# Optimization experiments

Measured on AMD Instinct MI355X. Metric: run time of the kernel, lower is better.

## Reference

```python
import jax, jax.numpy as jnp
import numpy as np

# Faithful emulation of SQBnBLinear: SmoothQuant rescale fused with
# bnb Linear8bitLt (threshold=0.0 => no fp16 outlier path):
#   w_sq = weight / scales ; x_sq = x * scales
#   row-wise absmax int8 quantization of both x (per token) and w (per out row)
#   int8 GEMM, then dequant with (ax * aw / 127^2), plus bias / scales.

B, S, D = 4, 2048, 4096

def setup_inputs() -> dict:
    key = jax.random.key(0)
    k1, k2, k3, k4 = jax.random.split(key, 4)
    x = jax.random.normal(k1, (B, S, D), dtype=jnp.float32)
    weight = jax.random.normal(k2, (D, D), dtype=jnp.float32) * 0.02
    bias = jax.random.normal(k3, (D,), dtype=jnp.float32) * 0.02
    # SmoothQuant scales are positive per-input-channel factors
    scales = jax.random.uniform(k4, (D,), dtype=jnp.float32, minval=0.5, maxval=2.0)
    return {"x": x, "weight": weight, "bias": bias, "scales": scales}

def _quantize_rowwise(t):
    # symmetric per-row (last-dim) absmax int8 quantization
    absmax = jnp.max(jnp.abs(t), axis=-1, keepdims=True)
    absmax = jnp.maximum(absmax, 1e-8)
    q = jnp.clip(jnp.round(t * (127.0 / absmax)), -127.0, 127.0)
    return q, absmax

def reference(x, weight, bias, scales):
    # __init__: fold SmoothQuant scales into weight and bias
    w_sq = weight / scales            # [out, in] / [in]
    b_sq = bias / scales              # valid because in_features == out_features
    # forward: rescale input (mul_ by scales)
    x_sq = x * scales                 # [B, S, in]
    # LLM.int8() with threshold=0.0: pure int8 path
    qx, ax = _quantize_rowwise(x_sq)  # qx [B,S,in], ax [B,S,1]
    qw, aw = _quantize_rowwise(w_sq)  # qw [out,in], aw [out,1]
    acc = jnp.einsum('bsi,oi->bso', qx, qw)  # int accumulate (emulated in fp32)
    out = acc * (ax / 127.0) * (aw[:, 0] / 127.0) + b_sq
    return out
```

## Files before the change

kernel.cpp:

```cpp
#include <hip/hip_runtime.h>
#include <stdint.h>

#define DDIM 4096
#define MTOK 8192

typedef __attribute__((ext_vector_type(4))) int i32x4;

__device__ __forceinline__ void async16(const void* g, void* l) {
    __builtin_amdgcn_global_load_lds(
        (const __attribute__((address_space(1))) unsigned int*)g,
        (__attribute__((address_space(3))) unsigned int*)l,
        16, 0, 0);
}

template <int MODE>
__global__ __launch_bounds__(256) void quant_rows(
    const float* __restrict__ src, const float* __restrict__ scales,
    signed char* __restrict__ q, float* __restrict__ srow,
    const float* __restrict__ bias, float* __restrict__ bq)
{
    __shared__ float red[4];
    const int row = blockIdx.x;
    const int tid = threadIdx.x;
    const float4* s4 = (const float4*)scales;
    const float4* x4 = (const float4*)(src + (size_t)row * DDIM);

    float4 v[4];
    float am = 0.0f;
#pragma unroll
    for (int j = 0; j < 4; ++j) {
        float4 a = x4[tid + j * 256];
        float4 s = s4[tid + j * 256];
        float4 r;
        if (MODE == 0) { r.x = a.x * s.x; r.y = a.y * s.y; r.z = a.z * s.z; r.w = a.w * s.w; }
        else           { r.x = a.x / s.x; r.y = a.y / s.y; r.z = a.z / s.z; r.w = a.w / s.w; }
        v[j] = r;
        am = fmaxf(am, fmaxf(fmaxf(fabsf(r.x), fabsf(r.y)),
                             fmaxf(fabsf(r.z), fabsf(r.w))));
    }
#pragma unroll
    for (int off = 32; off > 0; off >>= 1)
        am = fmaxf(am, __shfl_xor(am, off, 64));
    if ((tid & 63) == 0) red[tid >> 6] = am;
    __syncthreads();
    am = fmaxf(fmaxf(red[0], red[1]), fmaxf(red[2], red[3]));
    am = fmaxf(am, 1e-8f);

    const float sc = 127.0f / am;
    uint32_t* qrow = (uint32_t*)(q + (size_t)row * DDIM);
#pragma unroll
    for (int j = 0; j < 4; ++j) {
        int q0 = (int)fminf(127.0f, fmaxf(-127.0f, rintf(v[j].x * sc)));
        int q1 = (int)fminf(127.0f, fmaxf(-127.0f, rintf(v[j].y * sc)));
        int q2 = (int)fminf(127.0f, fmaxf(-127.0f, rintf(v[j].z * sc)));
        int q3 = (int)fminf(127.0f, fmaxf(-127.0f, rintf(v[j].w * sc)));
        qrow[tid + j * 256] = (uint32_t)(q0 & 0xff) | ((uint32_t)(q1 & 0xff) << 8) |
                              ((uint32_t)(q2 & 0xff) << 16) | ((uint32_t)(q3 & 0xff) << 24);
    }
    if (tid == 0) {
        srow[row] = am * (1.0f / 127.0f);
        if (MODE == 1) bq[row] = bias[row] / scales[row];
    }
}

__global__ __launch_bounds__(256) void gemm_i8(
    const signed char* __restrict__ qx, const signed char* __restrict__ qw,
    const float* __restrict__ sx, const float* __restrict__ sw,
    const float* __restrict__ bq, float* __restrict__ out)
{
    __shared__ __align__(16) signed char sA[128 * 64];
    __shared__ __align__(16) signed char sB[128 * 64];

    const int K = DDIM, N = DDIM;
    const int tid  = threadIdx.x;
    const int bm   = blockIdx.y;
    const int bn   = blockIdx.x;
    const int wave = tid >> 6;
    const int lane = tid & 63;
    const int wm   = (wave & 1) << 6;
    const int wn   = (wave >> 1) << 6;
    const int l16  = lane & 15;
    const int quad = lane >> 4;

    const signed char* Ab = qx + (size_t)bm * 128 * K;
    const signed char* Bb = qw + (size_t)bn * 128 * K;

    const int l0 = tid * 16;
    const int r0 = l0 >> 6, c0 = l0 & 63;
    const int l1 = l0 + 4096;
    const int r1 = l1 >> 6, c1 = l1 & 63;

    i32x4 acc[4][4] = {};

    for (int k0 = 0; k0 < K; k0 += 64) {
        async16(Ab + (size_t)r0 * K + k0 + c0, &sA[l0]);
        async16(Ab + (size_t)r1 * K + k0 + c1, &sA[l1]);
        async16(Bb + (size_t)r0 * K + k0 + c0, &sB[l0]);
        async16(Bb + (size_t)r1 * K + k0 + c1, &sB[l1]);
        __syncthreads();

        i32x4 a[4], b[4];
#pragma unroll
        for (int i = 0; i < 4; ++i)
            a[i] = *(const i32x4*)&sA[(wm + i * 16 + l16) * 64 + quad * 16];
#pragma unroll
        for (int j = 0; j < 4; ++j)
            b[j] = *(const i32x4*)&sB[(wn + j * 16 + l16) * 64 + quad * 16];

#pragma unroll
        for (int i = 0; i < 4; ++i)
#pragma unroll
            for (int j = 0; j < 4; ++j)
                acc[i][j] = __builtin_amdgcn_mfma_i32_16x16x64_i8(a[i], b[j], acc[i][j], 0, 0, 0);

        __syncthreads();
    }

#pragma unroll
    for (int i = 0; i < 4; ++i) {
#pragma unroll
        for (int j = 0; j < 4; ++j) {
            const int n = bn * 128 + wn + j * 16 + l16;
            const float swn = sw[n];
            const float bqn = bq[n];
#pragma unroll
            for (int r = 0; r < 4; ++r) {
                const int m = bm * 128 + wm + i * 16 + quad * 4 + r;
                out[(size_t)m * N + n] = (float)acc[i][j][r] * sx[m] * swn + bqn;
            }
        }
    }
}

extern "C" void kernel_launch(void* const* d_in, const int* in_sizes, int n_in,
                              void* d_out, int out_size, void* d_ws, size_t ws_size,
                              hipStream_t stream) {
    const float* x      = (const float*)d_in[0];
    const float* weight = (const float*)d_in[1];
    const float* bias   = (const float*)d_in[2];
    const float* scales = (const float*)d_in[3];
    float* out = (float*)d_out;

    char* ws = (char*)d_ws;
    signed char* qx = (signed char*)ws;
    signed char* qw = (signed char*)(ws + 33554432);
    float* sx = (float*)(ws + 50331648);
    float* sw = (float*)(ws + 50364416);
    float* bq = (float*)(ws + 50380800);

    quant_rows<0><<<MTOK, 256, 0, stream>>>(x, scales, qx, sx, nullptr, nullptr);
    quant_rows<1><<<DDIM, 256, 0, stream>>>(weight, scales, qw, sw, bias, bq);

    dim3 grid(DDIM / 128, MTOK / 128);
    gemm_i8<<<grid, 256, 0, stream>>>(qx, qw, sx, sw, bq, out);
}
```

Baseline: 439.3 us.

## Swizzle LDS layout for int8 GEMM tiles and merge quantization kernels

The GEMM now loads each 16-byte chunk from a global column chosen by XOR-ing the chunk index with row bits, so the shared-memory tile is stored swizzled. The MFMA fragment reads use the matching XOR, which is meant to cut LDS bank conflicts when lanes read 16-byte rows at a 64-byte stride. Separately, the activation and weight quantization kernels are merged into one launch covering both row sets, removing one launch and its tail. The merged kernel now decides multiply versus divide per block at run time instead of at compile time.

```diff
diff --git a/kernel.cpp b/kernel.cpp
--- a/kernel.cpp
+++ b/kernel.cpp
@@ -13,17 +13,23 @@
         16, 0, 0);
 }
 
-template <int MODE>
-__global__ __launch_bounds__(256) void quant_rows(
-    const float* __restrict__ src, const float* __restrict__ scales,
-    signed char* __restrict__ q, float* __restrict__ srow,
+__global__ __launch_bounds__(256) void quant_all(
+    const float* __restrict__ x, const float* __restrict__ weight,
+    const float* __restrict__ scales,
+    signed char* __restrict__ qx, float* __restrict__ sx,
+    signed char* __restrict__ qw, float* __restrict__ sw,
     const float* __restrict__ bias, float* __restrict__ bq)
 {
     __shared__ float red[4];
-    const int row = blockIdx.x;
     const int tid = threadIdx.x;
+    const bool is_x = blockIdx.x < MTOK;
+    const int row = is_x ? blockIdx.x : (blockIdx.x - MTOK);
+    const float* src = is_x ? (x + (size_t)row * DDIM) : (weight + (size_t)row * DDIM);
+    signed char* q = is_x ? qx : qw;
+    float* srow = is_x ? sx : sw;
+
     const float4* s4 = (const float4*)scales;
-    const float4* x4 = (const float4*)(src + (size_t)row * DDIM);
+    const float4* x4 = (const float4*)src;
 
     float4 v[4];
     float am = 0.0f;
@@ -32,8 +38,8 @@
         float4 a = x4[tid + j * 256];
         float4 s = s4[tid + j * 256];
         float4 r;
-        if (MODE == 0) { r.x = a.x * s.x; r.y = a.y * s.y; r.z = a.z * s.z; r.w = a.w * s.w; }
-        else           { r.x = a.x / s.x; r.y = a.y / s.y; r.z = a.z / s.z; r.w = a.w / s.w; }
+        if (is_x) { r.x = a.x * s.x; r.y = a.y * s.y; r.z = a.z * s.z; r.w = a.w * s.w; }
+        else      { r.x = a.x / s.x; r.y = a.y / s.y; r.z = a.z / s.z; r.w = a.w / s.w; }
         v[j] = r;
         am = fmaxf(am, fmaxf(fmaxf(fabsf(r.x), fabsf(r.y)),
                              fmaxf(fabsf(r.z), fabsf(r.w))));
@@ -59,7 +65,7 @@
     }
     if (tid == 0) {
         srow[row] = am * (1.0f / 127.0f);
-        if (MODE == 1) bq[row] = bias[row] / scales[row];
+        if (!is_x) bq[row] = bias[row] / scales[row];
     }
 }
 
@@ -86,26 +92,30 @@
     const signed char* Bb = qw + (size_t)bn * 128 * K;
 
     const int l0 = tid * 16;
-    const int r0 = l0 >> 6, c0 = l0 & 63;
+    const int r0 = l0 >> 6;
+    const int g0 = ((((l0 >> 4) & 3) ^ ((r0 >> 1) & 3)) << 4);
     const int l1 = l0 + 4096;
-    const int r1 = l1 >> 6, c1 = l1 & 63;
+    const int r1 = l1 >> 6;
+    const int g1 = ((((l1 >> 4) & 3) ^ ((r1 >> 1) & 3)) << 4);
+
+    const int rchunk = ((quad ^ ((l16 >> 1) & 3)) << 4);
 
     i32x4 acc[4][4] = {};
 
     for (int k0 = 0; k0 < K; k0 += 64) {
-        async16(Ab + (size_t)r0 * K + k0 + c0, &sA[l0]);
-        async16(Ab + (size_t)r1 * K + k0 + c1, &sA[l1]);
-        async16(Bb + (size_t)r0 * K + k0 + c0, &sB[l0]);
-        async16(Bb + (size_t)r1 * K + k0 + c1, &sB[l1]);
+        async16(Ab + (size_t)r0 * K + k0 + g0, &sA[l0]);
+        async16(Ab + (size_t)r1 * K + k0 + g1, &sA[l1]);
+        async16(Bb + (size_t)r0 * K + k0 + g0, &sB[l0]);
+        async16(Bb + (size_t)r1 * K + k0 + g1, &sB[l1]);
         __syncthreads();
 
         i32x4 a[4], b[4];
 #pragma unroll
         for (int i = 0; i < 4; ++i)
-            a[i] = *(const i32x4*)&sA[(wm + i * 16 + l16) * 64 + quad * 16];
+            a[i] = *(const i32x4*)&sA[(wm + i * 16 + l16) * 64 + rchunk];
 #pragma unroll
         for (int j = 0; j < 4; ++j)
-            b[j] = *(const i32x4*)&sB[(wn + j * 16 + l16) * 64 + quad * 16];
+            b[j] = *(const i32x4*)&sB[(wn + j * 16 + l16) * 64 + rchunk];
 
 #pragma unroll
         for (int i = 0; i < 4; ++i)
@@ -148,8 +158,7 @@
     float* sw = (float*)(ws + 50364416);
     float* bq = (float*)(ws + 50380800);
 
-    quant_rows<0><<<MTOK, 256, 0, stream>>>(x, scales, qx, sx, nullptr, nullptr);
-    quant_rows<1><<<DDIM, 256, 0, stream>>>(weight, scales, qw, sw, bias, bq);
+    quant_all<<<MTOK + DDIM, 256, 0, stream>>>(x, weight, scales, qx, sx, qw, sw, bias, bq);
 
     dim3 grid(DDIM / 128, MTOK / 128);
     gemm_i8<<<grid, 256, 0, stream>>>(qx, qw, sx, sw, bq, out);
```

Result: no change. 431.6 us (-1.7%).
